# Performance work log

Hardware: AMD Instinct MI355X
Metric: run time of the kernel (lower is better)

The kernel has to match this reference:

```python
import jax, jax.numpy as jnp
import numpy as np

D_MODEL = 1024
N_HEADS = 16
HEAD_DIM = D_MODEL // N_HEADS


def setup_inputs() -> dict:
    key = jax.random.key(0)
    k_x, k_wqkv, k_bqkv, k_wout, k_bout = jax.random.split(key, 5)
    s = 1.0 / np.sqrt(D_MODEL)
    return {
        "x": jax.random.normal(k_x, (4, 2048, D_MODEL), dtype=jnp.float32),
        "W_qkv": jax.random.normal(k_wqkv, (D_MODEL, 3 * D_MODEL), dtype=jnp.float32) * s,
        "b_qkv": jax.random.normal(k_bqkv, (3 * D_MODEL,), dtype=jnp.float32) * 0.01,
        "W_out": jax.random.normal(k_wout, (D_MODEL, D_MODEL), dtype=jnp.float32) * s,
        "b_out": jax.random.normal(k_bout, (D_MODEL,), dtype=jnp.float32) * 0.01,
    }


def reference(x, W_qkv, b_qkv, W_out, b_out):
    B, T, D = x.shape
    H, Hd = N_HEADS, HEAD_DIM
    qkv = x @ W_qkv + b_qkv                          # [B,T,3D]
    qkv = qkv.reshape(B, T, 3, H, Hd)
    q, k, v = (qkv[:, :, i].transpose(0, 2, 1, 3) for i in range(3))  # [B,H,T,Hd]
    scale = 1.0 / np.sqrt(Hd)
    attn = jnp.einsum("bhqd,bhkd->bhqk", q, k) * scale  # [B,H,T,T]
    causal = jnp.tril(jnp.ones((T, T), dtype=bool))
    attn = jnp.where(causal, attn, -jnp.inf)
    attn = jax.nn.softmax(attn, axis=-1)
    out = jnp.einsum("bhqk,bhkd->bhqd", attn, v)     # [B,H,T,Hd]
    out = out.transpose(0, 2, 1, 3).reshape(B, T, D)
    return out @ W_out + b_out
```

## Files before the change

### kernel.cpp

```cpp
#include <hip/hip_runtime.h>
#include <hip/hip_bf16.h>
#include <string.h>


typedef unsigned short u16;
typedef unsigned int u32;
typedef __bf16 bf16x8 __attribute__((ext_vector_type(8)));
typedef float f32x4 __attribute__((ext_vector_type(4)));

#define MFMA16(a, b, c) __builtin_amdgcn_mfma_f32_16x16x32_bf16((a), (b), (c), 0, 0, 0)

__device__ __forceinline__ u16 f2bf(float f) {
  unsigned u = __float_as_uint(f);
  u += 0x7fffu + ((u >> 16) & 1u);
  return (u16)(u >> 16);
}

__device__ __forceinline__ u32 pk2bf(float a, float b) {
  __hip_bfloat162 h = __float22bfloat162_rn(make_float2(a, b));
  u32 r;
  memcpy(&r, &h, 4);
  return r;
}

__device__ __forceinline__ void gload_lds16(const void* g, void* l) {
  __builtin_amdgcn_global_load_lds((const __attribute__((address_space(1))) void*)g,
                                   (__attribute__((address_space(3))) void*)l, 16, 0, 0);
}

__global__ __launch_bounds__(256) void cast_x_kernel(const float* __restrict__ x,
                                                     u16* __restrict__ xb) {
  int i = blockIdx.x * 256 + threadIdx.x;
  float4 v = ((const float4*)x)[i];
  ushort4 o;
  o.x = f2bf(v.x); o.y = f2bf(v.y); o.z = f2bf(v.z); o.w = f2bf(v.w);
  ((ushort4*)xb)[i] = o;
}

__global__ __launch_bounds__(256) void tcast_kernel(const float* __restrict__ W,
                                                    u16* __restrict__ Wt, int K, int N) {
  __shared__ float tile[32][33];
  int n0 = blockIdx.x * 32, k0 = blockIdx.y * 32;
  int tx = threadIdx.x & 31, ty = threadIdx.x >> 5;
#pragma unroll
  for (int i = 0; i < 4; i++) {
    int k = ty + i * 8;
    tile[k][tx] = W[(size_t)(k0 + k) * N + n0 + tx];
  }
  __syncthreads();
#pragma unroll
  for (int i = 0; i < 4; i++) {
    int n = ty + i * 8;
    Wt[(size_t)(n0 + n) * K + k0 + tx] = f2bf(tile[tx][n]);
  }
}

__global__ __launch_bounds__(256) void gemm_qkv_kernel(const u16* __restrict__ A,
                                                       const u16* __restrict__ Bt,
                                                       const float* __restrict__ bias,
                                                       u16* __restrict__ QKV) {
  __shared__ u16 As[128 * 32];
  __shared__ u16 Bs[128 * 32];
  const int tid = threadIdx.x, w = tid >> 6, lane = tid & 63;
  const int g = lane >> 4, c = lane & 15;
  const int wr = w >> 1, wc = w & 1;
  const int m0 = blockIdx.y * 128, n0 = blockIdx.x * 128;
  const int r4 = lane >> 2, c4 = lane & 3;

  f32x4 acc[4][4];
#pragma unroll
  for (int i = 0; i < 4; i++)
#pragma unroll
    for (int j = 0; j < 4; j++) acc[i][j] = (f32x4){0.f, 0.f, 0.f, 0.f};

  for (int k0 = 0; k0 < 1024; k0 += 32) {
    __syncthreads();
#pragma unroll
    for (int i = 0; i < 2; i++) {
      int rowb = w * 32 + i * 16;
      gload_lds16(A + (size_t)(m0 + rowb + r4) * 1024 + k0 + c4 * 8,
                  (char*)As + rowb * 64);
      gload_lds16(Bt + (size_t)(n0 + rowb + r4) * 1024 + k0 + c4 * 8,
                  (char*)Bs + rowb * 64);
    }
    __syncthreads();

    bf16x8 af[4], bf[4];
#pragma unroll
    for (int mt = 0; mt < 4; mt++)
      af[mt] = *(const bf16x8*)(As + (wr * 64 + mt * 16 + c) * 32 + g * 8);
#pragma unroll
    for (int nt = 0; nt < 4; nt++)
      bf[nt] = *(const bf16x8*)(Bs + (wc * 64 + nt * 16 + c) * 32 + g * 8);
#pragma unroll
    for (int mt = 0; mt < 4; mt++)
#pragma unroll
      for (int nt = 0; nt < 4; nt++) acc[mt][nt] = MFMA16(af[mt], bf[nt], acc[mt][nt]);
  }

  const float qscale = (n0 < 1024) ? 0.18033688011112042f : 1.0f;
  float bn[4];
#pragma unroll
  for (int nt = 0; nt < 4; nt++) bn[nt] = bias[n0 + wc * 64 + nt * 16 + c];
#pragma unroll
  for (int mt = 0; mt < 4; mt++) {
#pragma unroll
    for (int r = 0; r < 4; r++) {
      int m = m0 + wr * 64 + mt * 16 + g * 4 + r;
      int bb = m >> 11, t = m & 2047;
#pragma unroll
      for (int nt = 0; nt < 4; nt++) {
        int n = n0 + wc * 64 + nt * 16 + c;
        int which = n >> 10, rem = n & 1023, h = rem >> 6, d = rem & 63;
        float v = (acc[mt][nt][r] + bn[nt]) * qscale;
        QKV[(size_t)which * 8388608 + (((size_t)(bb * 16 + h) * 2048 + t) * 64 + d)] = f2bf(v);
      }
    }
  }
}

__global__ __launch_bounds__(256) void vtrans_kernel(const u16* __restrict__ V,
                                                     u16* __restrict__ Vt) {
  __shared__ u16 tile[64][65];
  int bh = blockIdx.y;
  int kt = blockIdx.x;
  int t0 = kt * 64;
  int tx = threadIdx.x & 63, ty = threadIdx.x >> 6;
  const u16* src = V + ((size_t)bh * 2048 + t0) * 64;
#pragma unroll
  for (int i = 0; i < 16; i++) {
    int tr = i * 4 + ty;
    tile[tr][tx] = src[tr * 64 + tx];
  }
  __syncthreads();
  u16* dst = Vt + ((size_t)(bh * 32 + kt)) * 4096;
#pragma unroll
  for (int i = 0; i < 16; i++) {
    int d = i * 4 + ty;
    dst[d * 64 + tx] = tile[tx][d];
  }
}

__global__ __launch_bounds__(512, 4) void attn_kernel(const u16* __restrict__ Q,
                                                      const u16* __restrict__ K,
                                                      const u16* __restrict__ Vt,
                                                      u16* __restrict__ ctx) {
  const int pr = blockIdx.x;
  const int qtA = pr, qtB = 15 - pr;
  const int h = blockIdx.y, b = blockIdx.z;
  const int bh = b * 16 + h;
  const int tid = threadIdx.x, w = tid >> 6, lane = tid & 63;
  const int g = lane >> 4, c = lane & 15;

  const u16* Kg = K + (size_t)bh * 2048 * 64;
  const u16* Vg = Vt + (size_t)bh * 32 * 4096;

  __shared__ u16 Ks[2][64 * 64];
  __shared__ u16 Vs[2][64 * 64];
  __shared__ u32 Pw[8][16 * 32];
  u32* pw = Pw[w];

  const int srow = lane >> 3;
  const int schunk = (lane & 7) ^ (srow & 7);
  const int cx = c & 7;
  const int off0 = ((g ^ cx) * 8);
  const int off1 = (((g ^ cx) ^ 4) * 8);
  const int sw = cx << 2;

  bf16x8 onesf;
#pragma unroll
  for (int i = 0; i < 8; i++) onesf[i] = (__bf16)1.0f;

  const u16* QgA = Q + ((size_t)bh * 2048 + qtA * 128) * 64;
  bf16x8 aq0 = *(const bf16x8*)(QgA + (w * 16 + c) * 64 + g * 8);
  bf16x8 aq1 = *(const bf16x8*)(QgA + (w * 16 + c) * 64 + 32 + g * 8);

  {
    int rbase = w * 8;
    gload_lds16(Kg + (size_t)(rbase + srow) * 64 + schunk * 8, (char*)(Ks[0]) + rbase * 128);
    gload_lds16(Vg + (size_t)(rbase + srow) * 64 + schunk * 8, (char*)(Vs[0]) + rbase * 128);
  }
  __syncthreads();

  f32x4 o[4], la;
#pragma unroll
  for (int nt = 0; nt < 4; nt++) o[nt] = (f32x4){0.f, 0.f, 0.f, 0.f};
  la = (f32x4){0.f, 0.f, 0.f, 0.f};

  const int nA = 2 * qtA + 2;

  auto store_tile = [&](int qbase) {
    float inv = 1.f / la[0];
    int q = qbase + w * 16 + c;
    size_t base = ((size_t)(b * 2048 + q)) * 1024 + h * 64;
#pragma unroll
    for (int nt = 0; nt < 4; nt++) {
      u32 lo = pk2bf(o[nt][0] * inv, o[nt][1] * inv);
      u32 hi = pk2bf(o[nt][2] * inv, o[nt][3] * inv);
      *(uint2*)(ctx + base + nt * 16 + g * 4) = make_uint2(lo, hi);
    }
  };

  for (int r = 0; r < 34; r++) {
    if (r) __syncthreads();

    if (r < 33) {
      const int ktn = (r + 1 < nA) ? (r + 1) : (r + 1 - nA);
      const int nb = (r + 1) & 1;
      int rbase = w * 8;
      gload_lds16(Kg + (size_t)ktn * 4096 + (size_t)(rbase + srow) * 64 + schunk * 8,
                  (char*)(Ks[nb]) + rbase * 128);
      gload_lds16(Vg + (size_t)ktn * 4096 + (size_t)(rbase + srow) * 64 + schunk * 8,
                  (char*)(Vs[nb]) + rbase * 128);
    }

    const bool inA = (r < nA);
    const int kt = inA ? r : (r - nA);
    const int qbase = inA ? qtA * 128 : qtB * 128;
    const int sb0 = qbase + w * 16;
    const int kb = kt * 64;

    if (kb <= sb0 + 15) {
      const u16* Kb = Ks[r & 1];
      const u16* Vb = Vs[r & 1];

      f32x4 sa[4];
#pragma unroll
      for (int nt = 0; nt < 4; nt++) {
        bf16x8 k0 = *(const bf16x8*)(Kb + (nt * 16 + c) * 64 + off0);
        bf16x8 k1 = *(const bf16x8*)(Kb + (nt * 16 + c) * 64 + off1);
        f32x4 z = (f32x4){0.f, 0.f, 0.f, 0.f};
        z = MFMA16(k0, aq0, z);
        z = MFMA16(k1, aq1, z);
        sa[nt] = z;
      }

      const bool domask = (kb + 63 > sb0);
      float pe[4][4];
#pragma unroll
      for (int nt = 0; nt < 4; nt++)
#pragma unroll
        for (int rr = 0; rr < 4; rr++) {
          float t = sa[nt][rr];
          if (domask && (kb + nt * 16 + g * 4 + rr) > (sb0 + c)) t = -1e30f;
          pe[nt][rr] = __builtin_amdgcn_exp2f(t);
        }
#pragma unroll
      for (int nt = 0; nt < 4; nt++) {
        u32 lo = pk2bf(pe[nt][0], pe[nt][1]);
        u32 hi = pk2bf(pe[nt][2], pe[nt][3]);
        *(uint2*)(pw + c * 32 + ((nt * 8 + g * 2) ^ sw)) = make_uint2(lo, hi);
      }
      bf16x8 pB0 = *(const bf16x8*)(pw + c * 32 + ((g * 4) ^ sw));
      bf16x8 pB1 = *(const bf16x8*)(pw + c * 32 + ((16 + g * 4) ^ sw));

      la = MFMA16(onesf, pB0, la);
      la = MFMA16(onesf, pB1, la);

#pragma unroll
      for (int nt = 0; nt < 4; nt++) {
        bf16x8 v0 = *(const bf16x8*)(Vb + (nt * 16 + c) * 64 + off0);
        bf16x8 v1 = *(const bf16x8*)(Vb + (nt * 16 + c) * 64 + off1);
        o[nt] = MFMA16(v0, pB0, o[nt]);
        o[nt] = MFMA16(v1, pB1, o[nt]);
      }
    }

    if (r == nA - 1) {
      store_tile(qtA * 128);
#pragma unroll
      for (int nt = 0; nt < 4; nt++) o[nt] = (f32x4){0.f, 0.f, 0.f, 0.f};
      la = (f32x4){0.f, 0.f, 0.f, 0.f};
      const u16* QgB = Q + ((size_t)bh * 2048 + qtB * 128) * 64;
      aq0 = *(const bf16x8*)(QgB + (w * 16 + c) * 64 + g * 8);
      aq1 = *(const bf16x8*)(QgB + (w * 16 + c) * 64 + 32 + g * 8);
    }
  }

  store_tile(qtB * 128);
}

__global__ __launch_bounds__(256) void gemm_proj_kernel(const u16* __restrict__ A,
                                                        const u16* __restrict__ Bt,
                                                        const float* __restrict__ bias,
                                                        float* __restrict__ out) {
  __shared__ u16 As[128 * 32];
  __shared__ u16 Bs[128 * 32];
  const int tid = threadIdx.x, w = tid >> 6, lane = tid & 63;
  const int g = lane >> 4, c = lane & 15;
  const int wr = w >> 1, wc = w & 1;
  const int m0 = blockIdx.y * 128, n0 = blockIdx.x * 128;
  const int r4 = lane >> 2, c4 = lane & 3;

  f32x4 acc[4][4];
#pragma unroll
  for (int i = 0; i < 4; i++)
#pragma unroll
    for (int j = 0; j < 4; j++) acc[i][j] = (f32x4){0.f, 0.f, 0.f, 0.f};

  for (int k0 = 0; k0 < 1024; k0 += 32) {
    __syncthreads();
#pragma unroll
    for (int i = 0; i < 2; i++) {
      int rowb = w * 32 + i * 16;
      gload_lds16(A + (size_t)(m0 + rowb + r4) * 1024 + k0 + c4 * 8,
                  (char*)As + rowb * 64);
      gload_lds16(Bt + (size_t)(n0 + rowb + r4) * 1024 + k0 + c4 * 8,
                  (char*)Bs + rowb * 64);
    }
    __syncthreads();

    bf16x8 af[4], bf[4];
#pragma unroll
    for (int mt = 0; mt < 4; mt++)
      af[mt] = *(const bf16x8*)(As + (wr * 64 + mt * 16 + c) * 32 + g * 8);
#pragma unroll
    for (int nt = 0; nt < 4; nt++)
      bf[nt] = *(const bf16x8*)(Bs + (wc * 64 + nt * 16 + c) * 32 + g * 8);
#pragma unroll
    for (int mt = 0; mt < 4; mt++)
#pragma unroll
      for (int nt = 0; nt < 4; nt++) acc[mt][nt] = MFMA16(af[mt], bf[nt], acc[mt][nt]);
  }

  float bn[4];
#pragma unroll
  for (int nt = 0; nt < 4; nt++) bn[nt] = bias[n0 + wc * 64 + nt * 16 + c];
#pragma unroll
  for (int mt = 0; mt < 4; mt++)
#pragma unroll
    for (int r = 0; r < 4; r++) {
      int m = m0 + wr * 64 + mt * 16 + g * 4 + r;
#pragma unroll
      for (int nt = 0; nt < 4; nt++) {
        int n = n0 + wc * 64 + nt * 16 + c;
        out[(size_t)m * 1024 + n] = acc[mt][nt][r] + bn[nt];
      }
    }
}

extern "C" void kernel_launch(void* const* d_in, const int* in_sizes, int n_in,
                              void* d_out, int out_size, void* d_ws, size_t ws_size,
                              hipStream_t stream) {
  const float* x = (const float*)d_in[0];
  const float* Wqkv = (const float*)d_in[1];
  const float* bqkv = (const float*)d_in[2];
  const float* Wout = (const float*)d_in[3];
  const float* bout = (const float*)d_in[4];
  float* out = (float*)d_out;

  char* ws = (char*)d_ws;
  u16* xb  = (u16*)(ws);
  u16* wqt = (u16*)(ws + 16777216);
  u16* wot = (u16*)(ws + 23068672);
  u16* Qb  = (u16*)(ws + 25165824);
  u16* Kb  = Qb + 8388608;
  u16* Vb  = Kb + 8388608;
  u16* Vt  = (u16*)(ws + 75497472);
  u16* ctx = (u16*)(ws + 92274688);

  cast_x_kernel<<<8192, 256, 0, stream>>>(x, xb);
  tcast_kernel<<<dim3(96, 32), 256, 0, stream>>>(Wqkv, wqt, 1024, 3072);
  tcast_kernel<<<dim3(32, 32), 256, 0, stream>>>(Wout, wot, 1024, 1024);
  gemm_qkv_kernel<<<dim3(24, 64), 256, 0, stream>>>(xb, wqt, bqkv, Qb);
  vtrans_kernel<<<dim3(32, 64), 256, 0, stream>>>(Vb, Vt);
  attn_kernel<<<dim3(8, 16, 4), 512, 0, stream>>>(Qb, Kb, Vt, ctx);
  gemm_proj_kernel<<<dim3(8, 64), 256, 0, stream>>>(ctx, wot, bout, out);
}
```

Baseline: 264.7 us.

## Triple-buffer attention K/V loads, permlane P transpose, setprio, XCD-swizzle GEMM tiles

The attention kernel moves from a double-buffered to a triple-buffered K/V ring. It prefetches two tiles ahead and waits with an explicit vmcnt plus a raw s_barrier instead of __syncthreads. The probability fragment is now rearranged with permlane32/16 swaps instead of a round trip through LDS, and the MFMA sections get raised wave priority. Both GEMM kernels remap the block index so neighbouring tiles are spread across the XCDs for better cache locality. The risks are extra LDS use, which may lower occupancy, and the correctness of the hand-written waitcnt and barrier synchronisation.

Measured after the change: 279.5 us. 1.06x slower.

```diff
diff --git a/kernel.cpp b/kernel.cpp
--- a/kernel.cpp
+++ b/kernel.cpp
@@ -7,6 +7,7 @@
 typedef unsigned int u32;
 typedef __bf16 bf16x8 __attribute__((ext_vector_type(8)));
 typedef float f32x4 __attribute__((ext_vector_type(4)));
+typedef unsigned int u32x2 __attribute__((ext_vector_type(2)));
 
 #define MFMA16(a, b, c) __builtin_amdgcn_mfma_f32_16x16x32_bf16((a), (b), (c), 0, 0, 0)
 
@@ -26,6 +27,18 @@
 __device__ __forceinline__ void gload_lds16(const void* g, void* l) {
   __builtin_amdgcn_global_load_lds((const __attribute__((address_space(1))) void*)g,
                                    (__attribute__((address_space(3))) void*)l, 16, 0, 0);
+}
+
+__device__ __forceinline__ u32x2 pl16swap(u32 a, u32 b) {
+  return __builtin_amdgcn_permlane16_swap(a, b, false, false);
+}
+__device__ __forceinline__ u32x2 pl32swap(u32 a, u32 b) {
+  return __builtin_amdgcn_permlane32_swap(a, b, false, false);
+}
+__device__ __forceinline__ bf16x8 mkfrag(u32 w0, u32 w1, u32 w2, u32 w3) {
+  union { u32 w[4]; bf16x8 v; } u;
+  u.w[0] = w0; u.w[1] = w1; u.w[2] = w2; u.w[3] = w3;
+  return u.v;
 }
 
 __global__ __launch_bounds__(256) void cast_x_kernel(const float* __restrict__ x,
@@ -64,7 +77,10 @@
   const int tid = threadIdx.x, w = tid >> 6, lane = tid & 63;
   const int g = lane >> 4, c = lane & 15;
   const int wr = w >> 1, wc = w & 1;
-  const int m0 = blockIdx.y * 128, n0 = blockIdx.x * 128;
+  const int nwg = gridDim.x * gridDim.y;
+  const int flat = blockIdx.y * gridDim.x + blockIdx.x;
+  const int swz = (flat & 7) * (nwg >> 3) + (flat >> 3);
+  const int m0 = (swz / gridDim.x) * 128, n0 = (swz % gridDim.x) * 128;
   const int r4 = lane >> 2, c4 = lane & 3;
 
   f32x4 acc[4][4];
@@ -155,17 +171,17 @@
   const u16* Kg = K + (size_t)bh * 2048 * 64;
   const u16* Vg = Vt + (size_t)bh * 32 * 4096;
 
-  __shared__ u16 Ks[2][64 * 64];
-  __shared__ u16 Vs[2][64 * 64];
-  __shared__ u32 Pw[8][16 * 32];
-  u32* pw = Pw[w];
+  __shared__ u16 Ks[3][64 * 64];
+  __shared__ u16 Vs[3][64 * 64];
 
   const int srow = lane >> 3;
   const int schunk = (lane & 7) ^ (srow & 7);
   const int cx = c & 7;
   const int off0 = ((g ^ cx) * 8);
   const int off1 = (((g ^ cx) ^ 4) * 8);
-  const int sw = cx << 2;
+  const int rbase = w * 8;
+  const u16* stK = Kg + (size_t)(rbase + srow) * 64 + schunk * 8;
+  const u16* stV = Vg + (size_t)(rbase + srow) * 64 + schunk * 8;
 
   bf16x8 onesf;
 #pragma unroll
@@ -175,12 +191,10 @@
   bf16x8 aq0 = *(const bf16x8*)(QgA + (w * 16 + c) * 64 + g * 8);
   bf16x8 aq1 = *(const bf16x8*)(QgA + (w * 16 + c) * 64 + 32 + g * 8);
 
-  {
-    int rbase = w * 8;
-    gload_lds16(Kg + (size_t)(rbase + srow) * 64 + schunk * 8, (char*)(Ks[0]) + rbase * 128);
-    gload_lds16(Vg + (size_t)(rbase + srow) * 64 + schunk * 8, (char*)(Vs[0]) + rbase * 128);
-  }
-  __syncthreads();
+  gload_lds16(stK, (char*)(Ks[0]) + rbase * 128);
+  gload_lds16(stV, (char*)(Vs[0]) + rbase * 128);
+  gload_lds16(stK + 4096, (char*)(Ks[1]) + rbase * 128);
+  gload_lds16(stV + 4096, (char*)(Vs[1]) + rbase * 128);
 
   f32x4 o[4], la;
 #pragma unroll
@@ -201,17 +215,23 @@
     }
   };
 
+  int cb = 0;
+
   for (int r = 0; r < 34; r++) {
-    if (r) __syncthreads();
-
     if (r < 33) {
-      const int ktn = (r + 1 < nA) ? (r + 1) : (r + 1 - nA);
-      const int nb = (r + 1) & 1;
-      int rbase = w * 8;
-      gload_lds16(Kg + (size_t)ktn * 4096 + (size_t)(rbase + srow) * 64 + schunk * 8,
-                  (char*)(Ks[nb]) + rbase * 128);
-      gload_lds16(Vg + (size_t)ktn * 4096 + (size_t)(rbase + srow) * 64 + schunk * 8,
-                  (char*)(Vs[nb]) + rbase * 128);
+      asm volatile("s_waitcnt vmcnt(2)" ::: "memory");
+    } else {
+      asm volatile("s_waitcnt vmcnt(0)" ::: "memory");
+    }
+    __builtin_amdgcn_s_barrier();
+    asm volatile("" ::: "memory");
+
+    if (r < 32) {
+      const int rr = r + 2;
+      const int ktn = (rr < nA) ? rr : rr - nA;
+      int pb = cb + 2; if (pb >= 3) pb -= 3;
+      gload_lds16(stK + (size_t)ktn * 4096, (char*)(Ks[pb]) + rbase * 128);
+      gload_lds16(stV + (size_t)ktn * 4096, (char*)(Vs[pb]) + rbase * 128);
     }
 
     const bool inA = (r < nA);
@@ -221,9 +241,10 @@
     const int kb = kt * 64;
 
     if (kb <= sb0 + 15) {
-      const u16* Kb = Ks[r & 1];
-      const u16* Vb = Vs[r & 1];
-
+      const u16* Kb = Ks[cb];
+      const u16* Vb = Vs[cb];
+
+      __builtin_amdgcn_s_setprio(1);
       f32x4 sa[4];
 #pragma unroll
       for (int nt = 0; nt < 4; nt++) {
@@ -234,6 +255,7 @@
         z = MFMA16(k1, aq1, z);
         sa[nt] = z;
       }
+      __builtin_amdgcn_s_setprio(0);
 
       const bool domask = (kb + 63 > sb0);
       float pe[4][4];
@@ -245,18 +267,27 @@
           if (domask && (kb + nt * 16 + g * 4 + rr) > (sb0 + c)) t = -1e30f;
           pe[nt][rr] = __builtin_amdgcn_exp2f(t);
         }
+
+      u32 wA[4], wB[4];
 #pragma unroll
       for (int nt = 0; nt < 4; nt++) {
-        u32 lo = pk2bf(pe[nt][0], pe[nt][1]);
-        u32 hi = pk2bf(pe[nt][2], pe[nt][3]);
-        *(uint2*)(pw + c * 32 + ((nt * 8 + g * 2) ^ sw)) = make_uint2(lo, hi);
+        wA[nt] = pk2bf(pe[nt][0], pe[nt][1]);
+        wB[nt] = pk2bf(pe[nt][2], pe[nt][3]);
       }
-      bf16x8 pB0 = *(const bf16x8*)(pw + c * 32 + ((g * 4) ^ sw));
-      bf16x8 pB1 = *(const bf16x8*)(pw + c * 32 + ((16 + g * 4) ^ sw));
-
+      u32x2 xa0 = pl32swap(wA[0], wA[1]);
+      u32x2 xb0 = pl32swap(wB[0], wB[1]);
+      u32x2 ya0 = pl16swap(xa0[0], xa0[1]);
+      u32x2 yb0 = pl16swap(xb0[0], xb0[1]);
+      bf16x8 pB0 = mkfrag(ya0[0], yb0[0], ya0[1], yb0[1]);
+      u32x2 xa1 = pl32swap(wA[2], wA[3]);
+      u32x2 xb1 = pl32swap(wB[2], wB[3]);
+      u32x2 ya1 = pl16swap(xa1[0], xa1[1]);
+      u32x2 yb1 = pl16swap(xb1[0], xb1[1]);
+      bf16x8 pB1 = mkfrag(ya1[0], yb1[0], ya1[1], yb1[1]);
+
+      __builtin_amdgcn_s_setprio(1);
       la = MFMA16(onesf, pB0, la);
       la = MFMA16(onesf, pB1, la);
-
 #pragma unroll
       for (int nt = 0; nt < 4; nt++) {
         bf16x8 v0 = *(const bf16x8*)(Vb + (nt * 16 + c) * 64 + off0);
@@ -264,6 +295,7 @@
         o[nt] = MFMA16(v0, pB0, o[nt]);
         o[nt] = MFMA16(v1, pB1, o[nt]);
       }
+      __builtin_amdgcn_s_setprio(0);
     }
 
     if (r == nA - 1) {
@@ -275,6 +307,8 @@
       aq0 = *(const bf16x8*)(QgB + (w * 16 + c) * 64 + g * 8);
       aq1 = *(const bf16x8*)(QgB + (w * 16 + c) * 64 + 32 + g * 8);
     }
+
+    cb++; if (cb == 3) cb = 0;
   }
 
   store_tile(qtB * 128);
@@ -289,7 +323,10 @@
   const int tid = threadIdx.x, w = tid >> 6, lane = tid & 63;
   const int g = lane >> 4, c = lane & 15;
   const int wr = w >> 1, wc = w & 1;
-  const int m0 = blockIdx.y * 128, n0 = blockIdx.x * 128;
+  const int nwg = gridDim.x * gridDim.y;
+  const int flat = blockIdx.y * gridDim.x + blockIdx.x;
+  const int swz = (flat & 7) * (nwg >> 3) + (flat >> 3);
+  const int m0 = (swz / gridDim.x) * 128, n0 = (swz % gridDim.x) * 128;
   const int r4 = lane >> 2, c4 = lane & 3;
 
   f32x4 acc[4][4];
```
